# Optimization experiments

Hardware: AMD Instinct MI355X
Metric: run time of the kernel (lower is better)

## Reference

```python
import jax, jax.numpy as jnp
import numpy as np

# ---- static radial-binning geometry for a 64x64 grid (classic azimuthalAverage) ----
_N = 64
_yy, _xx = np.indices((_N, _N))
_cx = (_xx.max() - _xx.min()) / 2.0  # 31.5
_cy = (_yy.max() - _yy.min()) / 2.0  # 31.5
_r = np.hypot(_xx - _cx, _yy - _cy)
_rint = _r.astype(int).ravel()                 # (4096,) integer radius per pixel
_NBINS = int(_rint.max()) + 1                  # 45 distinct integer radii (0..44)
_counts = np.bincount(_rint, minlength=_NBINS).astype(np.float32)
# classic azimuthalAverage (cumsum-of-sorted trick) returns bins 1 .. NBINS-2 inclusive
_ONEHOT = jnp.asarray(np.eye(_NBINS, dtype=np.float32)[_rint])  # (4096, 45) scatter matrix
_NR = jnp.asarray(_counts[1:_NBINS - 1])       # (43,) pixels per returned bin


def _tke(x):
    # x: (B, T, 2, 64, 64) -> turbulent kinetic energy (B, 64, 64)
    x = x.reshape(x.shape[0], -1, 2, _N, _N)
    mean_flow = jnp.mean(x, axis=1, keepdims=True)
    tur = jnp.mean((x - mean_flow) ** 2, axis=1)   # (B, 2, 64, 64) per-component variance
    return (tur[:, 0] + tur[:, 1]) * 0.5


def _spectrum(x):
    # TKE -> 2D power spectrum -> radial (azimuthal) average, all batched.
    tke = _tke(x)
    sp = jnp.fft.fftshift(jnp.fft.fft2(tke), axes=(-2, -1))
    power = jnp.real(sp * jnp.conj(sp)).reshape(x.shape[0], -1)  # (B, 4096)
    sums = power @ _ONEHOT                          # (B, 45) per-integer-radius sums
    return sums[:, 1:_NBINS - 1] / _NR              # (B, 43) azimuthal average


def setup_inputs() -> dict:
    key = jax.random.key(0)
    k1, k2 = jax.random.split(key)
    preds = jax.random.normal(k1, (64, 60, 2, 64, 64), dtype=jnp.float32)
    trues = jax.random.normal(k2, (64, 60, 2, 64, 64), dtype=jnp.float32)
    return {"preds": preds, "trues": trues}


def reference(preds, trues):
    # SpectrumLoss with loss = MSE: loss(tke2spectrum(trues), tke2spectrum(preds))
    sp_t = _spectrum(trues)
    sp_p = _spectrum(preds)
    return jnp.mean((sp_t - sp_p) ** 2)
```

## Files before the change

### kernel.cpp

```cpp
#include <hip/hip_runtime.h>
#include <math.h>

#define TT 60
#define BB 64
#define STR 68
#define NBINS 45

__global__ __launch_bounds__(256) void tke_kernel(const float* __restrict__ preds,
                                                  const float* __restrict__ trues,
                                                  float* __restrict__ tke) {
    int gtid = blockIdx.x * 256 + threadIdx.x;
    int input = gtid >> 16;
    int rem   = gtid & 65535;
    int b     = rem >> 10;
    int p4    = rem & 1023;
    const float4* src  = (const float4*)(input ? trues : preds);
    const float4* base = src + (size_t)b * (TT * 2 * 1024) + p4;
    float su[4]  = {0,0,0,0}, squ[4] = {0,0,0,0};
    float sv[4]  = {0,0,0,0}, sqv[4] = {0,0,0,0};
    #pragma unroll 4
    for (int t = 0; t < TT; ++t) {
        float4 u = base[t * 2048];
        float4 v = base[t * 2048 + 1024];
        float uu[4] = {u.x, u.y, u.z, u.w};
        float vv[4] = {v.x, v.y, v.z, v.w};
        #pragma unroll
        for (int j = 0; j < 4; ++j) {
            su[j]  += uu[j];  squ[j] += uu[j] * uu[j];
            sv[j]  += vv[j];  sqv[j] += vv[j] * vv[j];
        }
    }
    const float inv = 1.0f / 60.0f;
    float o[4];
    #pragma unroll
    for (int j = 0; j < 4; ++j) {
        float mu = su[j] * inv, mv = sv[j] * inv;
        o[j] = 0.5f * ((squ[j] * inv - mu * mu) + (sqv[j] * inv - mv * mv));
    }
    float4 outv; outv.x = o[0]; outv.y = o[1]; outv.z = o[2]; outv.w = o[3];
    ((float4*)tke)[(size_t)(input * BB + b) * 1024 + p4] = outv;
}

__global__ __launch_bounds__(512) void dft_kernel(const float* __restrict__ tke,
                                                  float* __restrict__ binsums) {
    __shared__ __align__(16) float tke_s[64 * 64];
    __shared__ __align__(16) float Gr[64 * STR];
    __shared__ __align__(16) float Gi[64 * STR];
    __shared__ float ctab[64], stab[64];
    __shared__ float bins_s[NBINS];

    int tid = threadIdx.x;
    int img = blockIdx.x;

    if (tid < 64) {
        float ang = (float)tid * 0.09817477042468103871f;
        float ss, cc;
        sincosf(ang, &ss, &cc);
        ctab[tid] = cc; stab[tid] = ss;
    }
    if (tid < NBINS) bins_s[tid] = 0.0f;

    {
        const float4* src = (const float4*)(tke + (size_t)img * 4096);
        float4* dst = (float4*)tke_s;
        for (int i = tid; i < 1024; i += 512) dst[i] = src[i];
    }
    __syncthreads();

    {
        int k  = tid >> 3;
        int x0 = (tid & 7) * 8;
        float gr[8] = {0,0,0,0,0,0,0,0};
        float gi[8] = {0,0,0,0,0,0,0,0};
        for (int y = 0; y < 64; ++y) {
            float4 ta = *(const float4*)&tke_s[(y << 6) + x0];
            float4 tb = *(const float4*)&tke_s[(y << 6) + x0 + 4];
            float tv[8] = {ta.x, ta.y, ta.z, ta.w, tb.x, tb.y, tb.z, tb.w};
            int idx = (k * y) & 63;
            float cc = ctab[idx], ss = stab[idx];
            #pragma unroll
            for (int j = 0; j < 8; ++j) {
                gr[j] += cc * tv[j];
                gi[j] -= ss * tv[j];
            }
        }
        #pragma unroll
        for (int j = 0; j < 8; ++j) {
            Gr[(x0 + j) * STR + k] = gr[j];
            Gi[(x0 + j) * STR + k] = gi[j];
        }
    }
    __syncthreads();

    {
        int l  = tid >> 3;
        int k0 = (tid & 7) * 8;
        float fr[8] = {0,0,0,0,0,0,0,0};
        float fi[8] = {0,0,0,0,0,0,0,0};
        for (int x = 0; x < 64; ++x) {
            float4 a0 = *(const float4*)&Gr[x * STR + k0];
            float4 a1 = *(const float4*)&Gr[x * STR + k0 + 4];
            float4 b0 = *(const float4*)&Gi[x * STR + k0];
            float4 b1 = *(const float4*)&Gi[x * STR + k0 + 4];
            float ar[8] = {a0.x, a0.y, a0.z, a0.w, a1.x, a1.y, a1.z, a1.w};
            float br[8] = {b0.x, b0.y, b0.z, b0.w, b1.x, b1.y, b1.z, b1.w};
            int idx = (l * x) & 63;
            float cc = ctab[idx], ss = stab[idx];
            #pragma unroll
            for (int j = 0; j < 8; ++j) {
                fr[j] += ar[j] * cc + br[j] * ss;
                fi[j] += br[j] * cc - ar[j] * ss;
            }
        }
        float fl = (float)((l + 32) & 63) - 31.5f;
        #pragma unroll
        for (int j = 0; j < 8; ++j) {
            int k = k0 + j;
            float fk = (float)((k + 32) & 63) - 31.5f;
            float r = sqrtf(fk * fk + fl * fl);
            int bin = (int)r;
            float pw = fr[j] * fr[j] + fi[j] * fi[j];
            atomicAdd(&bins_s[bin], pw);
        }
    }
    __syncthreads();
    if (tid < NBINS) binsums[img * NBINS + tid] = bins_s[tid];
}

__global__ __launch_bounds__(256) void loss_kernel(const float* __restrict__ binsums,
                                                   float* __restrict__ out) {
    __shared__ int   cnt[NBINS];
    __shared__ float part[256];
    int tid = threadIdx.x;
    if (tid < NBINS) cnt[tid] = 0;
    __syncthreads();
    for (int p = tid; p < 4096; p += 256) {
        float dy = (float)(p >> 6) - 31.5f;
        float dx = (float)(p & 63) - 31.5f;
        int bin = (int)sqrtf(dy * dy + dx * dx);
        atomicAdd(&cnt[bin], 1);
    }
    __syncthreads();
    float acc = 0.0f;
    for (int j = tid; j < BB * 43; j += 256) {
        int b   = j / 43;
        int bin = j - b * 43 + 1;
        float n  = (float)cnt[bin];
        float st = binsums[(BB + b) * NBINS + bin] / n;
        float sp = binsums[b * NBINS + bin] / n;
        float d  = st - sp;
        acc += d * d;
    }
    part[tid] = acc;
    __syncthreads();
    for (int s = 128; s > 0; s >>= 1) {
        if (tid < s) part[tid] += part[tid + s];
        __syncthreads();
    }
    if (tid == 0) out[0] = part[0] * (1.0f / (BB * 43.0f));
}

extern "C" void kernel_launch(void* const* d_in, const int* in_sizes, int n_in,
                              void* d_out, int out_size, void* d_ws, size_t ws_size,
                              hipStream_t stream) {
    const float* preds = (const float*)d_in[0];
    const float* trues = (const float*)d_in[1];
    float* tke     = (float*)d_ws;
    float* binsums = tke + 2 * BB * 4096;

    tke_kernel<<<512, 256, 0, stream>>>(preds, trues, tke);
    dft_kernel<<<128, 512, 0, stream>>>(tke, binsums);
    loss_kernel<<<1, 256, 0, stream>>>(binsums, (float*)d_out);
}
```

Measured before the change: 70.75 us.

## Split TKE time reduction across blocks with atomic staging and a finalize kernel

The per-pixel sum and sum-of-squares over 60 timesteps are split into four time quarters, each handled by its own 512-thread block. Partial sums are accumulated with global float atomics into a zeroed staging buffer. A separate finalize kernel then computes the variance into the TKE buffer. The aim is more memory-level parallelism and shorter serial loops in the bandwidth-heavy reduction, at the cost of a memset, millions of global atomics, an extra launch and extra staging traffic.

```diff
diff --git a/kernel.cpp b/kernel.cpp
--- a/kernel.cpp
+++ b/kernel.cpp
@@ -6,39 +6,82 @@
 #define STR 68
 #define NBINS 45
 
-__global__ __launch_bounds__(256) void tke_kernel(const float* __restrict__ preds,
-                                                  const float* __restrict__ trues,
-                                                  float* __restrict__ tke) {
-    int gtid = blockIdx.x * 256 + threadIdx.x;
-    int input = gtid >> 16;
-    int rem   = gtid & 65535;
-    int b     = rem >> 10;
-    int p4    = rem & 1023;
-    const float4* src  = (const float4*)(input ? trues : preds);
-    const float4* base = src + (size_t)b * (TT * 2 * 1024) + p4;
-    float su[4]  = {0,0,0,0}, squ[4] = {0,0,0,0};
-    float sv[4]  = {0,0,0,0}, sqv[4] = {0,0,0,0};
-    #pragma unroll 4
-    for (int t = 0; t < TT; ++t) {
-        float4 u = base[t * 2048];
-        float4 v = base[t * 2048 + 1024];
-        float uu[4] = {u.x, u.y, u.z, u.w};
-        float vv[4] = {v.x, v.y, v.z, v.w};
-        #pragma unroll
-        for (int j = 0; j < 4; ++j) {
-            su[j]  += uu[j];  squ[j] += uu[j] * uu[j];
-            sv[j]  += vv[j];  sqv[j] += vv[j] * vv[j];
-        }
-    }
+#define ACC1(S, Q, V) do {                                       \
+    S.x += V.x; Q.x += V.x * V.x;                                \
+    S.y += V.y; Q.y += V.y * V.y;                                \
+    S.z += V.z; Q.z += V.z * V.z;                                \
+    S.w += V.w; Q.w += V.w * V.w;                                \
+} while (0)
+
+__global__ __launch_bounds__(512, 4) void tke_partial(const float* __restrict__ preds,
+                                                      const float* __restrict__ trues,
+                                                      float* __restrict__ stage) {
+    int tid     = threadIdx.x;
+    int slab    = blockIdx.x;
+    int tensor  = slab >> 8;
+    int b       = (slab >> 2) & 63;
+    int quarter = slab & 3;
+
+    const float4* base = (const float4*)(tensor ? trues : preds)
+                         + (size_t)b * 122880 + (size_t)quarter * 30720 + tid;
+
+    float4 s0 = {0,0,0,0}, s1 = {0,0,0,0}, s2 = {0,0,0,0}, s3 = {0,0,0,0};
+    float4 q0 = {0,0,0,0}, q1 = {0,0,0,0}, q2 = {0,0,0,0}, q3 = {0,0,0,0};
+
+    for (int k = 0; k < 60; k += 4) {
+        float4 va = base[(k + 0) * 512];
+        float4 vb = base[(k + 1) * 512];
+        float4 vc = base[(k + 2) * 512];
+        float4 vd = base[(k + 3) * 512];
+        ACC1(s0, q0, va);
+        ACC1(s1, q1, vb);
+        ACC1(s2, q2, vc);
+        ACC1(s3, q3, vd);
+    }
+
+    size_t ib = (size_t)(tensor * BB + b);
+#define ATOM(S, Q, C, H) do {                                                         \
+    size_t fb = ((((ib * 2 + (C)) * 2 + 0) * 1024) + (size_t)(H) * 512 + tid) * 4;    \
+    size_t fq = fb + 4096;                                                            \
+    atomicAdd(&stage[fb + 0], S.x); atomicAdd(&stage[fb + 1], S.y);                   \
+    atomicAdd(&stage[fb + 2], S.z); atomicAdd(&stage[fb + 3], S.w);                   \
+    atomicAdd(&stage[fq + 0], Q.x); atomicAdd(&stage[fq + 1], Q.y);                   \
+    atomicAdd(&stage[fq + 2], Q.z); atomicAdd(&stage[fq + 3], Q.w);                   \
+} while (0)
+    ATOM(s0, q0, 0, 0);
+    ATOM(s1, q1, 0, 1);
+    ATOM(s2, q2, 1, 0);
+    ATOM(s3, q3, 1, 1);
+#undef ATOM
+}
+
+__global__ __launch_bounds__(256) void tke_final(const float* __restrict__ stage,
+                                                 float* __restrict__ tke) {
+    int gid    = blockIdx.x * 256 + threadIdx.x;
+    int tensor = gid >> 16;
+    int b      = (gid >> 10) & 63;
+    int p4     = gid & 1023;
+    size_t ib  = (size_t)(tensor * BB + b);
+
+    const float4* st = (const float4*)stage;
+    float4 su0 = st[((ib * 2 + 0) * 2 + 0) * 1024 + p4];
+    float4 sq0 = st[((ib * 2 + 0) * 2 + 1) * 1024 + p4];
+    float4 su1 = st[((ib * 2 + 1) * 2 + 0) * 1024 + p4];
+    float4 sq1 = st[((ib * 2 + 1) * 2 + 1) * 1024 + p4];
+
     const float inv = 1.0f / 60.0f;
-    float o[4];
-    #pragma unroll
-    for (int j = 0; j < 4; ++j) {
-        float mu = su[j] * inv, mv = sv[j] * inv;
-        o[j] = 0.5f * ((squ[j] * inv - mu * mu) + (sqv[j] * inv - mv * mv));
-    }
-    float4 outv; outv.x = o[0]; outv.y = o[1]; outv.z = o[2]; outv.w = o[3];
-    ((float4*)tke)[(size_t)(input * BB + b) * 1024 + p4] = outv;
+    float4 o;
+    {
+        float mu0 = su0.x * inv, mu1 = su1.x * inv;
+        o.x = 0.5f * ((sq0.x * inv - mu0 * mu0) + (sq1.x * inv - mu1 * mu1));
+        mu0 = su0.y * inv; mu1 = su1.y * inv;
+        o.y = 0.5f * ((sq0.y * inv - mu0 * mu0) + (sq1.y * inv - mu1 * mu1));
+        mu0 = su0.z * inv; mu1 = su1.z * inv;
+        o.z = 0.5f * ((sq0.z * inv - mu0 * mu0) + (sq1.z * inv - mu1 * mu1));
+        mu0 = su0.w * inv; mu1 = su1.w * inv;
+        o.w = 0.5f * ((sq0.w * inv - mu0 * mu0) + (sq1.w * inv - mu1 * mu1));
+    }
+    ((float4*)tke)[ib * 1024 + p4] = o;
 }
 
 __global__ __launch_bounds__(512) void dft_kernel(const float* __restrict__ tke,
@@ -165,10 +208,14 @@
                               hipStream_t stream) {
     const float* preds = (const float*)d_in[0];
     const float* trues = (const float*)d_in[1];
-    float* tke     = (float*)d_ws;
-    float* binsums = tke + 2 * BB * 4096;
-
-    tke_kernel<<<512, 256, 0, stream>>>(preds, trues, tke);
+
+    float* stage   = (float*)d_ws;
+    float* tke     = stage + 2097152;
+    float* binsums = tke + 524288;
+
+    hipMemsetAsync(stage, 0, 2097152 * sizeof(float), stream);
+    tke_partial<<<512, 512, 0, stream>>>(preds, trues, stage);
+    tke_final<<<512, 256, 0, stream>>>(stage, tke);
     dft_kernel<<<128, 512, 0, stream>>>(tke, binsums);
     loss_kernel<<<1, 256, 0, stream>>>(binsums, (float*)d_out);
 }
```

Result: slower. 175.8 us (+148.5%).
